# Kernel tuning notes

Hardware: AMD Instinct MI355X
Metric: run time of the kernel (lower is better)

Reference implementation:

```python
import jax, jax.numpy as jnp
import numpy as np

HEADS = 4


def setup_inputs() -> dict:
    key = jax.random.key(0)
    kx, kqkv, kbq, ko, kbo = jax.random.split(key, 5)
    B, C, H, W = 4, 256, 64, 64
    x = jax.random.normal(kx, (B, C, H, W), dtype=jnp.float32)
    # torch nn.Linear stores weight as [out_features, in_features]
    w_qkv = jax.random.normal(kqkv, (3 * C, C), dtype=jnp.float32) * (1.0 / np.sqrt(C))
    b_qkv = jax.random.normal(kbq, (3 * C,), dtype=jnp.float32) * 0.02
    w_o = jax.random.normal(ko, (C, C), dtype=jnp.float32) * (1.0 / np.sqrt(C))
    b_o = jax.random.normal(kbo, (C,), dtype=jnp.float32) * 0.02
    return {"x": x, "w_qkv": w_qkv, "b_qkv": b_qkv, "w_o": w_o, "b_o": b_o}


def reference(x, w_qkv, b_qkv, w_o, b_o):
    B, C, H, W = x.shape
    S = H * W
    hd = C // HEADS
    # (B, C, H, W) -> (B, S, C)
    xt = x.reshape(B, C, S).transpose(0, 2, 1)
    qkv = xt @ w_qkv.T + b_qkv                      # (B, S, 3C)
    q, k, v = jnp.split(qkv, 3, axis=-1)
    def to_heads(t):
        return t.reshape(B, S, HEADS, hd).transpose(0, 2, 1, 3)  # (B, h, S, hd)
    q, k, v = to_heads(q), to_heads(k), to_heads(v)
    scores = jnp.einsum('bhqd,bhkd->bhqk', q, k) / jnp.sqrt(jnp.float32(hd))
    attn = jax.nn.softmax(scores, axis=-1)          # dropout inactive (eval)
    out = jnp.einsum('bhqk,bhkd->bhqd', attn, v)    # (B, h, S, hd)
    out = out.transpose(0, 2, 1, 3).reshape(B, S, C)
    y = out @ w_o.T + b_o                            # (B, S, C)
    y = y.reshape(B, H, W, C).transpose(0, 3, 1, 2)  # (B, C, H, W)
    return y
```

## Files before the change

kernel.cpp:

```cpp
#include <hip/hip_runtime.h>
#include <stdint.h>

#define DI __device__ __forceinline__

typedef __attribute__((ext_vector_type(8))) __bf16 bf16x8;
typedef __attribute__((ext_vector_type(8))) unsigned short u16x8;
typedef __attribute__((ext_vector_type(4))) float f32x4;
typedef __attribute__((ext_vector_type(4))) uint32_t u32x4;
typedef unsigned short u16;

constexpr int Bb = 4, Cc = 256, Ss = 4096, HD = 64;
constexpr int ELEMS = Bb * Cc * Ss;

DI float bf2f(u16 h) { union { unsigned u; float f; } x; x.u = ((unsigned)h) << 16; return x.f; }
DI u16 f2bf(float f) {
  union { float f; unsigned u; } x; x.f = f;
  return (u16)((x.u + 0x7FFFu + ((x.u >> 16) & 1u)) >> 16);
}
DI uint32_t pack2bf_trunc(float a, float b) {
  union { float f; uint32_t u; } xa, xb;
  xa.f = a; xb.f = b;
  return __builtin_amdgcn_perm(xb.u, xa.u, 0x07060302u);
}
DI bf16x8 ldfrag(const u16* p) { return __builtin_bit_cast(bf16x8, *(const u16x8*)p); }

DI void g2l16(const u16* g, u16* l) {
  __builtin_amdgcn_global_load_lds((const __attribute__((address_space(1))) uint32_t*)(const void*)g,
                                   (__attribute__((address_space(3))) uint32_t*)(void*)l, 16, 0, 0);
}

__global__ __launch_bounds__(256) void k_transpose(const float* __restrict__ x, u16* __restrict__ xt,
                                                   const float* __restrict__ wq, const float* __restrict__ wo,
                                                   u16* __restrict__ wqb, u16* __restrict__ wob) {
  __shared__ u16 T[64][72];
  const int st = blockIdx.x, ct = blockIdx.y, b = blockIdx.z;
  const int tid = threadIdx.x;
  {
    int flat = blockIdx.x + 64 * blockIdx.y + 256 * blockIdx.z;
    int widx = flat * 256 + tid;
    if (widx < 196608) wqb[widx] = f2bf(wq[widx]);
    else wob[widx - 196608] = f2bf(wo[widx - 196608]);
  }
#pragma unroll
  for (int e = 0; e < 2; e++) {
    int ss = tid + e * 256;
    int r = ss >> 3, seg = ss & 7;
    size_t base = ((size_t)(b * Cc + ct * 64 + r) << 12) + st * 64 + seg * 8;
    const float4* xv = (const float4*)(x + base);
    float4 v0 = xv[0], v1 = xv[1];
    u16x8 t;
    t[0] = f2bf(v0.x); t[1] = f2bf(v0.y); t[2] = f2bf(v0.z); t[3] = f2bf(v0.w);
    t[4] = f2bf(v1.x); t[5] = f2bf(v1.y); t[6] = f2bf(v1.z); t[7] = f2bf(v1.w);
    *(u16x8*)&T[r][(seg ^ ((r >> 3) & 7)) * 8] = t;
  }
  __syncthreads();
#pragma unroll
  for (int e = 0; e < 2; e++) {
    int ss = tid + e * 256;
    int sr = ss >> 3, cseg = ss & 7;
    u16x8 o;
#pragma unroll
    for (int j = 0; j < 8; j++) {
      int row = cseg * 8 + j;
      o[j] = T[row][(((sr >> 3) ^ cseg) * 8) + (sr & 7)];
    }
    *(u16x8*)(xt + ((size_t)(b * Ss + st * 64 + sr) << 8) + ct * 64 + cseg * 8) = o;
  }
}

DI void stage_tile(const u16* __restrict__ src, int pitch, int r0, int k0, u16 (*dst)[40], int tid) {
#pragma unroll
  for (int e = 0; e < 2; e++) {
    int c = tid + e * 256;
    int row = c >> 2, seg = c & 3;
    u16x8 t = *(const u16x8*)(src + (size_t)(r0 + row) * pitch + k0 + seg * 8);
    *(u16x8*)&dst[row][seg * 8] = t;
  }
}

__global__ __launch_bounds__(256) void k_qkv(const u16* __restrict__ xt, const u16* __restrict__ w,
                                             const float* __restrict__ bias,
                                             u16* __restrict__ q, u16* __restrict__ kk_, u16* __restrict__ vt) {
  __shared__ union {
    u16 ab[2][128][40];
    u16 tile[128][136];
  } sm;
  const int tid = threadIdx.x;
  const int wv = tid >> 6, lane = tid & 63;
  const int wm = wv >> 1, wn = wv & 1;
  const int lr = lane & 15, quad = lane >> 4;
  const int r0 = blockIdx.x * 128;
  const int j0 = blockIdx.y * 128;
  f32x4 acc[4][4] = {};
  for (int k0 = 0; k0 < 256; k0 += 32) {
    __syncthreads();
    stage_tile(xt, 256, r0, k0, sm.ab[0], tid);
    stage_tile(w, 256, j0, k0, sm.ab[1], tid);
    __syncthreads();
    bf16x8 a[4], b[4];
#pragma unroll
    for (int mt = 0; mt < 4; mt++) a[mt] = ldfrag(&sm.ab[0][wm * 64 + mt * 16 + lr][quad * 8]);
#pragma unroll
    for (int nt = 0; nt < 4; nt++) b[nt] = ldfrag(&sm.ab[1][wn * 64 + nt * 16 + lr][quad * 8]);
#pragma unroll
    for (int mt = 0; mt < 4; mt++)
#pragma unroll
      for (int nt = 0; nt < 4; nt++)
        acc[mt][nt] = __builtin_amdgcn_mfma_f32_16x16x32_bf16(a[mt], b[nt], acc[mt][nt], 0, 0, 0);
  }
  float bj[4];
#pragma unroll
  for (int nt = 0; nt < 4; nt++) bj[nt] = bias[j0 + wn * 64 + nt * 16 + lr];
  __syncthreads();
  if (blockIdx.y < 4) {
    const int part = blockIdx.y >> 1;
    u16* outp = part ? kk_ : q;
    const float sc = part ? 1.0f : 0.18033688f;
#pragma unroll
    for (int nt = 0; nt < 4; nt++) {
      int lc = wn * 64 + nt * 16 + lr;
#pragma unroll
      for (int mt = 0; mt < 4; mt++)
#pragma unroll
        for (int rg = 0; rg < 4; rg++)
          sm.tile[wm * 64 + mt * 16 + quad * 4 + rg][lc] = f2bf((acc[mt][nt][rg] + bj[nt]) * sc);
    }
    __syncthreads();
    const int hb2 = (blockIdx.y & 1) * 2;
#pragma unroll
    for (int it = 0; it < 8; it++) {
      int seg = tid + it * 256;
      int row = seg >> 4, cs = seg & 15;
      u16x8 o = *(const u16x8*)&sm.tile[row][cs * 8];
      int head = hb2 + (cs >> 3), d0 = (cs & 7) * 8;
      int rr = r0 + row, b_ = rr >> 12, s = rr & 4095;
      *(u16x8*)(outp + ((size_t)((b_ * 4 + head) * Ss + s) << 6) + d0) = o;
    }
  } else {
    const int hb = (blockIdx.y - 4) * 2;
#pragma unroll
    for (int nt = 0; nt < 4; nt++) {
      int lc = wn * 64 + nt * 16 + lr;
#pragma unroll
      for (int mt = 0; mt < 4; mt++)
#pragma unroll
        for (int rg = 0; rg < 4; rg++)
          sm.tile[wm * 64 + mt * 16 + quad * 4 + rg][lc] = f2bf(acc[mt][nt][rg] + bj[nt]);
    }
    __syncthreads();
    const int b2 = r0 >> 12, sbase = r0 & 4095;
#pragma unroll
    for (int it = 0; it < 8; it++) {
      int seg = tid + it * 256;
      int sq = seg & 15, hd = seg >> 4;
      int c = sq >> 3, s8 = sq & 7;
      u16x8 o;
#pragma unroll
      for (int j = 0; j < 8; j++) {
        int slot = s8 * 8 + j;
        int sw = (((slot >> 5) & 1) << 5) | (((slot >> 2) & 1) << 4) |
                 (((slot >> 3) & 3) << 2) | (slot & 3);
        o[j] = sm.tile[c * 64 + sw][hd];
      }
      int head = hb + (hd >> 6), d = hd & 63;
      *(u16x8*)(vt + ((size_t)((b2 * 4 + head) * 64 + d) << 12) + sbase + c * 64 + s8 * 8) = o;
    }
  }
}

__global__ __launch_bounds__(512, 4) void k_attn(const u16* __restrict__ Q, const u16* __restrict__ K,
                                                 const u16* __restrict__ VT, u16* __restrict__ AO,
                                                 u16* __restrict__ AOP, float* __restrict__ lpart,
                                                 int nsplit) {
  __shared__ u16 Kl[2][2][64][64];
  __shared__ u16 Vl[2][2][64][64];
  const int tid = threadIdx.x;
  const int wv = tid >> 6, lane = tid & 63;
  const int lr = lane & 15, quad = lane >> 4;
  const int bh = blockIdx.y;
  const int b_ = bh >> 2, head = bh & 3;
  const int qbase = blockIdx.x * 256 + wv * 32;
  const int sp = blockIdx.z;
  const int nbig = 32 / nsplit, bg0 = sp * nbig;
  const u16* Qh = Q + (size_t)bh * Ss * HD;
  const u16* Kh = K + (size_t)bh * Ss * HD;
  const u16* Vh = VT + (size_t)bh * HD * Ss;

  bf16x8 qb[2][2];
#pragma unroll
  for (int nt = 0; nt < 2; nt++)
#pragma unroll
    for (int ks = 0; ks < 2; ks++)
      qb[nt][ks] = ldfrag(Qh + (size_t)(qbase + nt * 16 + lr) * HD + ks * 32 + quad * 8);

  u16x8 ov;
#pragma unroll
  for (int j = 0; j < 8; j++) ov[j] = 0x3F80;
  const bf16x8 ones = __builtin_bit_cast(bf16x8, ov);

  f32x4 O[2][4] = {};
  f32x4 lacc[2] = {};

  const int srow = wv * 8 + (lane >> 3);
  const int sseg = ((lane & 7) ^ (lane >> 3)) * 8;
  const u16* pK = Kh + ((size_t)(bg0 * 128 + srow) << 6) + sseg;
  const u16* pV = Vh + ((size_t)srow << 12) + bg0 * 128 + sseg;
  auto stage = [&](int buf) {
#pragma unroll
    for (int s = 0; s < 2; s++) {
      g2l16(pK + (s << 12), &Kl[buf][s][wv * 8][0]);
      g2l16(pV + s * 64, &Vl[buf][s][wv * 8][0]);
    }
    pK += 8192; pV += 128;
  };

  stage(0);
  __syncthreads();

  for (int bc = 0; bc < nbig; bc++) {
    const int cur = bc & 1;
    if (bc + 1 < nbig) stage(cur ^ 1);

#pragma unroll
    for (int sub = 0; sub < 2; sub++) {
      u32x4 pa[2][2];
#pragma unroll
      for (int t = 0; t < 4; t++) {
        const int krow = t * 16 + lr;
        bf16x8 ka0 = ldfrag(&Kl[cur][sub][krow][(quad ^ (lr & 7)) * 8]);
        bf16x8 ka1 = ldfrag(&Kl[cur][sub][krow][((4 + quad) ^ (lr & 7)) * 8]);
        f32x4 St[2] = {};
        __builtin_amdgcn_s_setprio(1);
#pragma unroll
        for (int nt = 0; nt < 2; nt++)
          St[nt] = __builtin_amdgcn_mfma_f32_16x16x32_bf16(ka0, qb[nt][0], St[nt], 0, 0, 0);
#pragma unroll
        for (int nt = 0; nt < 2; nt++)
          St[nt] = __builtin_amdgcn_mfma_f32_16x16x32_bf16(ka1, qb[nt][1], St[nt], 0, 0, 0);
        __builtin_amdgcn_s_setprio(0);
        const int h = t >> 1, k2 = (t & 1) * 2;
#pragma unroll
        for (int nt = 0; nt < 2; nt++) {
          float p0 = __builtin_amdgcn_exp2f(St[nt][0]);
          float p1 = __builtin_amdgcn_exp2f(St[nt][1]);
          float p2 = __builtin_amdgcn_exp2f(St[nt][2]);
          float p3 = __builtin_amdgcn_exp2f(St[nt][3]);
          pa[h][nt][k2] = pack2bf_trunc(p0, p1);
          pa[h][nt][k2 + 1] = pack2bf_trunc(p2, p3);
        }
      }
#pragma unroll
      for (int h = 0; h < 2; h++) {
#pragma unroll
        for (int dt = 0; dt < 4; dt++) {
          bf16x8 vb = ldfrag(&Vl[cur][sub][dt * 16 + lr][((h * 4 + quad) ^ (lr & 7)) * 8]);
          __builtin_amdgcn_s_setprio(1);
#pragma unroll
          for (int mt = 0; mt < 2; mt++)
            O[mt][dt] = __builtin_amdgcn_mfma_f32_16x16x32_bf16(
                __builtin_bit_cast(bf16x8, pa[h][mt]), vb, O[mt][dt], 0, 0, 0);
          __builtin_amdgcn_s_setprio(0);
        }
#pragma unroll
        for (int mt = 0; mt < 2; mt++)
          lacc[mt] = __builtin_amdgcn_mfma_f32_16x16x32_bf16(
              __builtin_bit_cast(bf16x8, pa[h][mt]), ones, lacc[mt], 0, 0, 0);
      }
    }
    __syncthreads();
  }

  u16* dst = (nsplit == 1) ? AO : (AOP + (size_t)sp * ELEMS);
  if (nsplit > 1 && lr == 0) {
    float* lp = lpart + (size_t)sp * (16 * Ss) + bh * Ss;
#pragma unroll
    for (int mt = 0; mt < 2; mt++)
#pragma unroll
      for (int rg = 0; rg < 4; rg++) lp[qbase + mt * 16 + quad * 4 + rg] = lacc[mt][rg];
  }
#pragma unroll
  for (int mt = 0; mt < 2; mt++)
#pragma unroll
    for (int rg = 0; rg < 4; rg++) {
      float inv = 1.0f / lacc[mt][rg];
      int s = qbase + mt * 16 + quad * 4 + rg;
#pragma unroll
      for (int dt = 0; dt < 4; dt++)
        dst[((size_t)(b_ * Ss + s) << 8) + head * 64 + dt * 16 + lr] = f2bf(O[mt][dt][rg] * inv);
    }
}

__global__ __launch_bounds__(256) void k_oproj(const u16* __restrict__ wo, const u16* __restrict__ ao,
                                               const u16* __restrict__ AOP, const float* __restrict__ lpart,
                                               const float* __restrict__ bo, float* __restrict__ y, int nsplit) {
  __shared__ u16 As[128][40], Bs[64][40];
  const int tid = threadIdx.x;
  const int wv = tid >> 6, lane = tid & 63;
  const int wm = wv >> 1, wn = wv & 1;
  const int lr = lane & 15, quad = lane >> 4;
  const int n0 = blockIdx.x * 64;
  const int m0 = blockIdx.y * 128;
  f32x4 acc[4][2] = {};
  for (int k0 = 0; k0 < 256; k0 += 32) {
    __syncthreads();
    stage_tile(wo, 256, m0, k0, As, tid);
    {
      int row = tid >> 2, seg = tid & 3;
      int bs = n0 + row, cc = k0 + seg * 8;
      u16x8 t;
      if (nsplit == 1) {
        t = *(const u16x8*)(ao + ((size_t)bs << 8) + cc);
      } else {
        int b = bs >> 12, s = bs & 4095, head = cc >> 6;
        int li = (b * 4 + head) * Ss + s;
        float accv[8] = {0.f, 0.f, 0.f, 0.f, 0.f, 0.f, 0.f, 0.f};
        float lsum = 0.f;
        for (int spl = 0; spl < nsplit; spl++) {
          float l = lpart[(size_t)spl * (16 * Ss) + li];
          u16x8 a = *(const u16x8*)(AOP + (size_t)spl * ELEMS + ((size_t)bs << 8) + cc);
          lsum += l;
#pragma unroll
          for (int i = 0; i < 8; i++) accv[i] += l * bf2f(a[i]);
        }
        float inv = 1.0f / lsum;
#pragma unroll
        for (int i = 0; i < 8; i++) t[i] = f2bf(accv[i] * inv);
      }
      *(u16x8*)&Bs[row][seg * 8] = t;
    }
    __syncthreads();
    bf16x8 a[4], b[2];
#pragma unroll
    for (int mt = 0; mt < 4; mt++) a[mt] = ldfrag(&As[wm * 64 + mt * 16 + lr][quad * 8]);
#pragma unroll
    for (int nt = 0; nt < 2; nt++) b[nt] = ldfrag(&Bs[wn * 32 + nt * 16 + lr][quad * 8]);
#pragma unroll
    for (int mt = 0; mt < 4; mt++)
#pragma unroll
      for (int nt = 0; nt < 2; nt++)
        acc[mt][nt] = __builtin_amdgcn_mfma_f32_16x16x32_bf16(a[mt], b[nt], acc[mt][nt], 0, 0, 0);
  }
#pragma unroll
  for (int mt = 0; mt < 4; mt++)
#pragma unroll
    for (int rg = 0; rg < 4; rg++) {
      int c = m0 + wm * 64 + mt * 16 + quad * 4 + rg;
      float bc = bo[c];
#pragma unroll
      for (int nt = 0; nt < 2; nt++) {
        int col = n0 + wn * 32 + nt * 16 + lr;
        int b_ = col >> 12, s = col & 4095;
        y[((size_t)(b_ * Cc + c) << 12) + s] = acc[mt][nt][rg] + bc;
      }
    }
}

extern "C" void kernel_launch(void* const* d_in, const int* in_sizes, int n_in,
                              void* d_out, int out_size, void* d_ws, size_t ws_size,
                              hipStream_t stream) {
  const float* x = (const float*)d_in[0];
  const float* w_qkv = (const float*)d_in[1];
  const float* b_qkv = (const float*)d_in[2];
  const float* w_o = (const float*)d_in[3];
  const float* b_o = (const float*)d_in[4];
  float* y = (float*)d_out;
  u16* ws = (u16*)d_ws;
  u16* xt = ws;
  u16* q = ws + (size_t)ELEMS;
  u16* k = ws + (size_t)2 * ELEMS;
  u16* vt = ws + (size_t)3 * ELEMS;
  u16* ao = xt;
  u16* wqb = ws + (size_t)4 * ELEMS;
  u16* wob = wqb + 196608;
  const size_t Wu16 = (size_t)4 * ELEMS + 262144;
  auto need = [&](int n) { return (Wu16 + (size_t)n * ELEMS) * 2 + (size_t)n * 16 * Ss * 4; };
  const int nsplit = (ws_size >= need(2)) ? 2 : 1;
  u16* aop = ws + Wu16;
  float* lpart = (float*)(aop + (size_t)nsplit * ELEMS);

  k_transpose<<<dim3(64, 4, 4), 256, 0, stream>>>(x, xt, w_qkv, w_o, wqb, wob);
  k_qkv<<<dim3(128, 6), 256, 0, stream>>>(xt, wqb, b_qkv, q, k, vt);
  k_attn<<<dim3(16, 16, nsplit), 512, 0, stream>>>(q, k, vt, ao, aop, lpart, nsplit);
  k_oproj<<<dim3(256, 2), 256, 0, stream>>>(wob, ao, aop, lpart, b_o, y, nsplit);
}
```

Measured before the change: 172.3 us.

## Use direct global-to-LDS loads with double buffering and XOR swizzle in projections

Replaces register-staged tile copies in the QKV and output projection GEMMs with direct global-to-LDS 16-byte loads (g2l16). The QKV GEMM gains double-buffered shared tiles so the next K-slice loads while MFMAs run on the current one, with one barrier per step. Padded LDS rows are replaced by an XOR swizzle on the 8-element segment to avoid bank conflicts. The aim is to cut VGPR traffic and barrier stalls, at the cost of relying on the g2l16 helper and swizzle indexing being correct.

```diff
diff --git a/kernel.cpp b/kernel.cpp
--- a/kernel.cpp
+++ b/kernel.cpp
@@ -68,21 +68,11 @@
   }
 }
 
-DI void stage_tile(const u16* __restrict__ src, int pitch, int r0, int k0, u16 (*dst)[40], int tid) {
-#pragma unroll
-  for (int e = 0; e < 2; e++) {
-    int c = tid + e * 256;
-    int row = c >> 2, seg = c & 3;
-    u16x8 t = *(const u16x8*)(src + (size_t)(r0 + row) * pitch + k0 + seg * 8);
-    *(u16x8*)&dst[row][seg * 8] = t;
-  }
-}
-
 __global__ __launch_bounds__(256) void k_qkv(const u16* __restrict__ xt, const u16* __restrict__ w,
                                              const float* __restrict__ bias,
                                              u16* __restrict__ q, u16* __restrict__ kk_, u16* __restrict__ vt) {
   __shared__ union {
-    u16 ab[2][128][40];
+    u16 ab[2][2][128][32];
     u16 tile[128][136];
   } sm;
   const int tid = threadIdx.x;
@@ -91,23 +81,45 @@
   const int lr = lane & 15, quad = lane >> 4;
   const int r0 = blockIdx.x * 128;
   const int j0 = blockIdx.y * 128;
+
+  const int srow = lane >> 2;
+  const int sg = ((lane & 3) ^ (srow & 3)) * 8;
+  const u16* pA[2];
+  const u16* pB[2];
+#pragma unroll
+  for (int e = 0; e < 2; e++) {
+    pA[e] = xt + (size_t)(r0 + e * 64 + wv * 16 + srow) * 256 + sg;
+    pB[e] = w + (size_t)(j0 + e * 64 + wv * 16 + srow) * 256 + sg;
+  }
+  auto stage = [&](int buf, int k0) {
+#pragma unroll
+    for (int e = 0; e < 2; e++) {
+      g2l16(pA[e] + k0, &sm.ab[buf][0][e * 64 + wv * 16][0]);
+      g2l16(pB[e] + k0, &sm.ab[buf][1][e * 64 + wv * 16][0]);
+    }
+  };
+
   f32x4 acc[4][4] = {};
-  for (int k0 = 0; k0 < 256; k0 += 32) {
-    __syncthreads();
-    stage_tile(xt, 256, r0, k0, sm.ab[0], tid);
-    stage_tile(w, 256, j0, k0, sm.ab[1], tid);
-    __syncthreads();
+  stage(0, 0);
+  __syncthreads();
+  for (int ks = 0; ks < 8; ks++) {
+    const int cur = ks & 1;
+    if (ks < 7) stage(cur ^ 1, (ks + 1) * 32);
     bf16x8 a[4], b[4];
 #pragma unroll
-    for (int mt = 0; mt < 4; mt++) a[mt] = ldfrag(&sm.ab[0][wm * 64 + mt * 16 + lr][quad * 8]);
-#pragma unroll
-    for (int nt = 0; nt < 4; nt++) b[nt] = ldfrag(&sm.ab[1][wn * 64 + nt * 16 + lr][quad * 8]);
+    for (int mt = 0; mt < 4; mt++)
+      a[mt] = ldfrag(&sm.ab[cur][0][wm * 64 + mt * 16 + lr][(quad ^ (lr & 3)) * 8]);
+#pragma unroll
+    for (int nt = 0; nt < 4; nt++)
+      b[nt] = ldfrag(&sm.ab[cur][1][wn * 64 + nt * 16 + lr][(quad ^ (lr & 3)) * 8]);
 #pragma unroll
     for (int mt = 0; mt < 4; mt++)
 #pragma unroll
       for (int nt = 0; nt < 4; nt++)
         acc[mt][nt] = __builtin_amdgcn_mfma_f32_16x16x32_bf16(a[mt], b[nt], acc[mt][nt], 0, 0, 0);
-  }
+    __syncthreads();
+  }
+
   float bj[4];
 #pragma unroll
   for (int nt = 0; nt < 4; nt++) bj[nt] = bias[j0 + wn * 64 + nt * 16 + lr];
@@ -293,17 +305,24 @@
 __global__ __launch_bounds__(256) void k_oproj(const u16* __restrict__ wo, const u16* __restrict__ ao,
                                                const u16* __restrict__ AOP, const float* __restrict__ lpart,
                                                const float* __restrict__ bo, float* __restrict__ y, int nsplit) {
-  __shared__ u16 As[128][40], Bs[64][40];
+  __shared__ u16 As[128][32], Bs[64][40];
   const int tid = threadIdx.x;
   const int wv = tid >> 6, lane = tid & 63;
   const int wm = wv >> 1, wn = wv & 1;
   const int lr = lane & 15, quad = lane >> 4;
   const int n0 = blockIdx.x * 64;
   const int m0 = blockIdx.y * 128;
+  const int srow = lane >> 2;
+  const int sg = ((lane & 3) ^ (srow & 3)) * 8;
+  const u16* pA[2];
+#pragma unroll
+  for (int e = 0; e < 2; e++)
+    pA[e] = wo + (size_t)(m0 + e * 64 + wv * 16 + srow) * 256 + sg;
   f32x4 acc[4][2] = {};
   for (int k0 = 0; k0 < 256; k0 += 32) {
     __syncthreads();
-    stage_tile(wo, 256, m0, k0, As, tid);
+#pragma unroll
+    for (int e = 0; e < 2; e++) g2l16(pA[e] + k0, &As[e * 64 + wv * 16][0]);
     {
       int row = tid >> 2, seg = tid & 3;
       int bs = n0 + row, cc = k0 + seg * 8;
@@ -331,7 +350,8 @@
     __syncthreads();
     bf16x8 a[4], b[2];
 #pragma unroll
-    for (int mt = 0; mt < 4; mt++) a[mt] = ldfrag(&As[wm * 64 + mt * 16 + lr][quad * 8]);
+    for (int mt = 0; mt < 4; mt++)
+      a[mt] = ldfrag(&As[wm * 64 + mt * 16 + lr][(quad ^ (lr & 3)) * 8]);
 #pragma unroll
     for (int nt = 0; nt < 2; nt++) b[nt] = ldfrag(&Bs[wn * 32 + nt * 16 + lr][quad * 8]);
 #pragma unroll
```

Result: faster. 167.9 us (-2.6%).
